# Performance work log

Measured on AMD Instinct MI355X. Metric: run time of the kernel, lower is better.

## Reference

```python
import jax, jax.numpy as jnp
import numpy as np

TOP_K = 1024  # init top_k


def setup_inputs() -> dict:
    key = jax.random.key(0)
    ks = jax.random.split(key, 11)
    B, S, D, H = 8, 1024, 1024, 4096
    s = 0.02
    return {
        "inputs": jax.random.normal(ks[0], (B, S, D), jnp.float32),
        "up_w": jax.random.normal(ks[1], (H, D), jnp.float32) * s,
        "up_b": jax.random.normal(ks[2], (H,), jnp.float32) * s,
        "gate_w1": jax.random.normal(ks[3], (H, D), jnp.float32) * s,
        "gate_b1": jax.random.normal(ks[4], (H,), jnp.float32) * s,
        "gate_w2": jax.random.normal(ks[5], (H, H), jnp.float32) * s,
        "gate_b2": jax.random.normal(ks[6], (H,), jnp.float32) * s,
        "mod_w": jax.random.normal(ks[7], (H, D), jnp.float32) * s,
        "mod_b": jax.random.normal(ks[8], (H,), jnp.float32) * s,
        "down_w": jax.random.normal(ks[9], (D, H), jnp.float32) * s,
        "down_b": jax.random.normal(ks[10], (D,), jnp.float32) * s,
    }


def reference(inputs, up_w, up_b, gate_w1, gate_b1, gate_w2, gate_b2,
              mod_w, mod_b, down_w, down_b):
    B, S, D = inputs.shape
    H = up_w.shape[0]
    # gate: Linear -> ReLU -> Linear, scores [B,S,H]
    scores = jax.nn.relu(jnp.einsum('bsd,hd->bsh', inputs, gate_w1) + gate_b1)
    scores = jnp.einsum('bsh,gh->bsg', scores, gate_w2) + gate_b2
    flat_scores = scores.reshape(B, S * H)
    k = min(TOP_K * S, S * H)
    _, flat_idx = jax.lax.top_k(flat_scores, k)          # [B,k]
    hidden_idx = flat_idx % H                            # [B,k]
    # scatter writes mod.weight[h] at row h -> duplicates harmless -> boolean mask
    batch_idx = jnp.broadcast_to(jnp.arange(B)[:, None], (B, k))
    mask = jnp.zeros((B, H), bool).at[batch_idx, hidden_idx].set(True)
    # per-batch modified weights/bias (materialized like torch repeat+index_put)
    w = jnp.where(mask[:, :, None], mod_w[None], up_w[None])   # [B,H,D]
    b = jnp.where(mask, mod_b[None], up_b[None])               # [B,H]
    h = jnp.einsum('bsd,bhd->bsh', inputs, w) + b[:, None, :]
    h = jax.nn.silu(h)
    # dropout p=0.0 (eval) -> identity
    return jnp.einsum('bsh,dh->bsd', h, down_w) + down_b
```

## Files before the change

### kernel.cpp

```cpp
#include <hip/hip_runtime.h>
#include <cstdint>

typedef __attribute__((ext_vector_type(8))) short short8;
typedef __attribute__((ext_vector_type(4))) float floatx4;
typedef unsigned int uint32;

typedef const void __attribute__((address_space(1)))* gcptr;
typedef void __attribute__((address_space(3)))* lptr;

constexpr int Bn = 8, Sn = 1024, Dn = 1024, Hn = 4096;
constexpr uint32 KTOP = 1024u * 1024u;
constexpr uint32 SKBASE = 0xBB000000u;
constexpr uint32 EMAX = (1u << 27) - 1u;
constexpr uint32 WLO = 3645;
constexpr uint32 WHI = 4157;
constexpr uint32 CAP = 1u << 20;

constexpr size_t NX  = (size_t)Bn * Sn * Dn;
constexpr size_t NW1 = (size_t)Hn * Dn;
constexpr size_t NW2 = (size_t)Hn * Hn;
constexpr size_t NRS = (size_t)Bn * Sn * Hn;

constexpr size_t OFF_XH   = 0;
constexpr size_t OFF_XL   = OFF_XH  + 2 * NX;
constexpr size_t OFF_W1H  = OFF_XL  + 2 * NX;
constexpr size_t OFF_W1L  = OFF_W1H + 2 * NW1;
constexpr size_t OFF_W2H  = OFF_W1L + 2 * NW1;
constexpr size_t OFF_W2L  = OFF_W2H + 2 * NW2;
constexpr size_t OFF_RSH  = OFF_W2L + 2 * NW2;
constexpr size_t OFF_RSL  = OFF_RSH + 2 * NRS;
constexpr size_t OFF_HIST = OFF_RSL + 2 * NRS;
constexpr size_t OFF_HIST2= OFF_HIST + (size_t)Bn * 8192 * 4;
constexpr size_t OFF_HMAX = OFF_HIST2+ (size_t)Bn * 16384 * 4;
constexpr size_t OFF_META = OFF_HMAX + (size_t)Bn * Hn * 4;
constexpr size_t OFF_BSEL = OFF_META + 4096;
constexpr size_t OFF_MASK = OFF_BSEL + (size_t)Bn * Hn * 4;
constexpr size_t WS_SMALL = OFF_MASK + (size_t)Bn * Hn * 4;
constexpr size_t ZERO_BYTES = OFF_BSEL - OFF_HIST;
constexpr size_t OFF_BUF  = OFF_XL;

#define VMCNT(n) asm volatile("s_waitcnt vmcnt(" #n ")" ::: "memory")

__device__ __forceinline__ ushort f2bf(float f) {
  uint32 u = __float_as_uint(f);
  u += 0x7fffu + ((u >> 16) & 1u);
  return (ushort)(u >> 16);
}
__device__ __forceinline__ float bf2f(ushort h) {
  return __uint_as_float(((uint32)h) << 16);
}
__device__ __forceinline__ uint32 skey(float v) {
  uint32 u = __float_as_uint(v);
  return (u & 0x80000000u) ? ~u : (u | 0x80000000u);
}
__device__ __forceinline__ uint32 ekey(uint32 key) {
  if (key <= SKBASE) return 0u;
  uint32 d = key - SKBASE;
  return d > EMAX ? EMAX : d;
}
__device__ __forceinline__ void g2l(const ushort* src, ushort* dst) {
  __builtin_amdgcn_global_load_lds((gcptr)src, (lptr)dst, 16, 0, 0);
}
__device__ __forceinline__ void stage_tile(ushort* lds, const ushort* gbase, int ldg, int tid) {
  const int w = tid >> 6;
  const int c0 = tid, c1 = tid + 256;
  g2l(gbase + (size_t)(c0 >> 2) * ldg + (c0 & 3) * 8, lds + (size_t)(w * 64) * 8);
  g2l(gbase + (size_t)(c1 >> 2) * ldg + (c1 & 3) * 8, lds + (size_t)(256 + w * 64) * 8);
}

__global__ __launch_bounds__(256) void cvt_split_k(const float4* __restrict__ x,
                                                   ushort* __restrict__ hi,
                                                   ushort* __restrict__ lo, int n4) {
  int stride = gridDim.x * 256;
  for (int i = blockIdx.x * 256 + threadIdx.x; i < n4; i += stride) {
    float4 v = x[i];
    ushort h0 = f2bf(v.x), h1 = f2bf(v.y), h2 = f2bf(v.z), h3 = f2bf(v.w);
    ushort4 hv; hv.x = h0; hv.y = h1; hv.z = h2; hv.w = h3;
    *(ushort4*)(hi + (size_t)i * 4) = hv;
    ushort4 lv;
    lv.x = f2bf(v.x - bf2f(h0)); lv.y = f2bf(v.y - bf2f(h1));
    lv.z = f2bf(v.z - bf2f(h2)); lv.w = f2bf(v.w - bf2f(h3));
    *(ushort4*)(lo + (size_t)i * 4) = lv;
  }
}
__global__ __launch_bounds__(256) void cvt_single_k(const float4* __restrict__ x,
                                                    ushort* __restrict__ hi, int n4) {
  int stride = gridDim.x * 256;
  for (int i = blockIdx.x * 256 + threadIdx.x; i < n4; i += stride) {
    float4 v = x[i];
    ushort4 hv; hv.x = f2bf(v.x); hv.y = f2bf(v.y); hv.z = f2bf(v.z); hv.w = f2bf(v.w);
    *(ushort4*)(hi + (size_t)i * 4) = hv;
  }
}
__global__ __launch_bounds__(256) void zero_out_k(float* __restrict__ o, int n) {
  int i = blockIdx.x * 256 + threadIdx.x;
  if (i < n) o[i] = 0.f;
}

constexpr int EPI_RELU = 0;
constexpr int EPI_SCORE = 1;
constexpr int EPI_SILU = 2;
constexpr int EPI_F32 = 3;

template <bool SPLIT, bool SELB, int EPI>
__global__ __launch_bounds__(256, SPLIT ? 3 : 2) void gemm_bt(
    const ushort* __restrict__ Ah, const ushort* __restrict__ Al,
    const ushort* __restrict__ Bh, const ushort* __restrict__ Bl,
    const uint32* __restrict__ bmask,
    int N, int K, long long a_bs, long long o_bs, long long bias_bs,
    const float* __restrict__ bias,
    void* __restrict__ outp, void* __restrict__ out2p) {
  __shared__ __align__(16) ushort lds[SPLIT ? 16384 : 8192];
  ushort* As = lds;
  ushort* Bs = lds + (SPLIT ? 8192 : 4096);

  const int tid = threadIdx.x;
  const int w = tid >> 6, l = tid & 63;
  const int wm = (w >> 1) << 6, wn = (w & 1) << 6;
  const int lm = l & 15, lq = l >> 4;
  const int m0 = blockIdx.y << 7, n0 = blockIdx.x << 7;
  const int z = blockIdx.z;

  const ushort* pAh = Ah + (size_t)z * a_bs + (size_t)m0 * K;
  const ushort* pBh = Bh + (size_t)n0 * K;

  floatx4 acc[4][4];
#pragma unroll
  for (int i = 0; i < 4; i++)
#pragma unroll
    for (int j = 0; j < 4; j++) acc[i][j] = floatx4{0.f, 0.f, 0.f, 0.f};

  for (int k0 = 0; k0 < K; k0 += 32) {
    stage_tile(As, pAh + k0, K, tid);
    stage_tile(Bs, pBh + k0, K, tid);
    __syncthreads();
    short8 afh[4], bfh[4];
#pragma unroll
    for (int i = 0; i < 4; i++)
      afh[i] = *(const short8*)&As[(wm + i * 16 + lm) * 32 + lq * 8];
#pragma unroll
    for (int i = 0; i < 4; i++)
      bfh[i] = *(const short8*)&Bs[(wn + i * 16 + lm) * 32 + lq * 8];
#pragma unroll
    for (int mi = 0; mi < 4; mi++)
#pragma unroll
      for (int ni = 0; ni < 4; ni++)
        acc[mi][ni] = __builtin_amdgcn_mfma_f32_16x16x32_bf16(afh[mi], bfh[ni], acc[mi][ni], 0, 0, 0);
    __syncthreads();
  }

  if constexpr (EPI == EPI_SILU) {
    ushort* o = (ushort*)outp + (size_t)z * o_bs;
    const float* bb = bias + (size_t)z * bias_bs;
#pragma unroll
    for (int mi = 0; mi < 4; mi++)
#pragma unroll
      for (int ni = 0; ni < 4; ni++) {
        int gm = m0 + wm + mi * 16 + lq * 4;
        int gn = n0 + wn + ni * 16 + lm;
        float bnv = bb[gn];
#pragma unroll
        for (int r = 0; r < 4; r++) {
          float v = acc[mi][ni][r] + bnv;
          float s = v / (1.f + __expf(-v));
          o[(size_t)(gm + r) * N + gn] = f2bf(s);
        }
      }
  } else if constexpr (EPI == EPI_F32) {
    float* o = (float*)outp;
#pragma unroll
    for (int mi = 0; mi < 4; mi++)
#pragma unroll
      for (int ni = 0; ni < 4; ni++) {
        int gm = m0 + wm + mi * 16 + lq * 4;
        int gn = n0 + wn + ni * 16 + lm;
        float bnv = bias[gn];
#pragma unroll
        for (int r = 0; r < 4; r++)
          o[(size_t)(gm + r) * N + gn] = acc[mi][ni][r] + bnv;
      }
  }
}

__device__ __forceinline__ short8 fragld(const ushort* S, int r, int swz) {
  return *(const short8*)&S[r * 32 + swz];
}
__device__ __forceinline__ void mfma_block(floatx4 (&acc)[8][4], const short8 (&af)[4],
                                           int mi0, const short8 (&bf)[4]) {
#pragma unroll
  for (int mi = 0; mi < 4; mi++)
#pragma unroll
    for (int ni = 0; ni < 4; ni++)
      acc[mi0 + mi][ni] =
          __builtin_amdgcn_mfma_f32_16x16x32_bf16(af[mi], bf[ni], acc[mi0 + mi][ni], 0, 0, 0);
}

template <bool ST>
__device__ __forceinline__ void kstep_sp(
    floatx4 (&acc)[8][4], ushort* ldsb, int p, int ko,
    const ushort* sAh0, const ushort* sAh1, const ushort* sBh0, const ushort* sBh1,
    const ushort* sAl0, const ushort* sAl1, const ushort* sBl0, const ushort* sBl1,
    int dbase, int swz, int lm, int wrow, int wcol) {
  const ushort* AhS = ldsb + (p * 4 + 0) * 8192;
  const ushort* BhS = ldsb + (p * 4 + 1) * 8192;
  const ushort* AlS = ldsb + (p * 4 + 2) * 8192;
  const ushort* BlS = ldsb + (p * 4 + 3) * 8192;
  ushort* dAh = ldsb + ((p ^ 1) * 4 + 0) * 8192;
  ushort* dBh = ldsb + ((p ^ 1) * 4 + 1) * 8192;
  ushort* dAl = ldsb + ((p ^ 1) * 4 + 2) * 8192;
  ushort* dBl = ldsb + ((p ^ 1) * 4 + 3) * 8192;

  short8 ahT[4], ahB[4], bh[4], bl[4];
#pragma unroll
  for (int i = 0; i < 4; i++) ahT[i] = fragld(AhS, wrow + i * 16 + lm, swz);
#pragma unroll
  for (int i = 0; i < 4; i++) bh[i]  = fragld(BhS, wcol + i * 16 + lm, swz);
#pragma unroll
  for (int i = 0; i < 4; i++) ahB[i] = fragld(AhS, wrow + 64 + i * 16 + lm, swz);
  if constexpr (ST) { g2l(sAh0 + ko, dAh + dbase); g2l(sAh1 + ko, dAh + dbase + 4096); }
  __builtin_amdgcn_s_barrier();
  __builtin_amdgcn_s_setprio(1);
  mfma_block(acc, ahT, 0, bh);
  __builtin_amdgcn_s_setprio(0);
  if constexpr (ST) VMCNT(2); else VMCNT(0);
  __builtin_amdgcn_s_barrier();
#pragma unroll
  for (int i = 0; i < 4; i++) bl[i] = fragld(BlS, wcol + i * 16 + lm, swz);
  if constexpr (ST) { g2l(sBh0 + ko, dBh + dbase); g2l(sBh1 + ko, dBh + dbase + 4096); }
  __builtin_amdgcn_s_barrier();
  __builtin_amdgcn_s_setprio(1);
  mfma_block(acc, ahB, 4, bh);
  __builtin_amdgcn_s_setprio(0);
  __builtin_amdgcn_s_barrier();
  if constexpr (ST) { g2l(sAl0 + ko, dAl + dbase); g2l(sAl1 + ko, dAl + dbase + 4096); }
  __builtin_amdgcn_s_barrier();
  __builtin_amdgcn_s_setprio(1);
  mfma_block(acc, ahT, 0, bl);
  __builtin_amdgcn_s_setprio(0);
  __builtin_amdgcn_s_barrier();
  short8 alT[4];
#pragma unroll
  for (int i = 0; i < 4; i++) alT[i] = fragld(AlS, wrow + i * 16 + lm, swz);
  if constexpr (ST) { g2l(sBl0 + ko, dBl + dbase); g2l(sBl1 + ko, dBl + dbase + 4096); }
  __builtin_amdgcn_s_barrier();
  __builtin_amdgcn_s_setprio(1);
  mfma_block(acc, ahB, 4, bl);
  __builtin_amdgcn_s_setprio(0);
  __builtin_amdgcn_s_barrier();
  short8 alB[4];
#pragma unroll
  for (int i = 0; i < 4; i++) alB[i] = fragld(AlS, wrow + 64 + i * 16 + lm, swz);
  __builtin_amdgcn_s_barrier();
  __builtin_amdgcn_s_setprio(1);
  mfma_block(acc, alT, 0, bh);
  __builtin_amdgcn_s_setprio(0);
  __builtin_amdgcn_s_barrier();
  __builtin_amdgcn_s_setprio(1);
  mfma_block(acc, alB, 4, bh);
  __builtin_amdgcn_s_setprio(0);
  if constexpr (ST) VMCNT(4);
  __builtin_amdgcn_s_barrier();
}

template <bool ST>
__device__ __forceinline__ void kstep_ns(
    floatx4 (&acc)[8][4], ushort* ldsb, int p, int ko,
    const ushort* sA0, const ushort* sA1, const ushort* sB0, const ushort* sB1,
    int dbase, int swz, int lm, int wrow, int wcol) {
  const ushort* AS = ldsb + (p * 2 + 0) * 8192;
  const ushort* BS = ldsb + (p * 2 + 1) * 8192;
  ushort* dA = ldsb + ((p ^ 1) * 2 + 0) * 8192;
  ushort* dB = ldsb + ((p ^ 1) * 2 + 1) * 8192;
  short8 aT[4], aB[4], b[4];
#pragma unroll
  for (int i = 0; i < 4; i++) aT[i] = fragld(AS, wrow + i * 16 + lm, swz);
#pragma unroll
  for (int i = 0; i < 4; i++) b[i]  = fragld(BS, wcol + i * 16 + lm, swz);
#pragma unroll
  for (int i = 0; i < 4; i++) aB[i] = fragld(AS, wrow + 64 + i * 16 + lm, swz);
  if constexpr (ST) {
    g2l(sA0 + ko, dA + dbase); g2l(sA1 + ko, dA + dbase + 4096);
    g2l(sB0 + ko, dB + dbase); g2l(sB1 + ko, dB + dbase + 4096);
  }
  __builtin_amdgcn_s_barrier();
  __builtin_amdgcn_s_setprio(1);
  mfma_block(acc, aT, 0, b);
  __builtin_amdgcn_s_setprio(0);
  __builtin_amdgcn_s_barrier();
  __builtin_amdgcn_s_setprio(1);
  mfma_block(acc, aB, 4, b);
  __builtin_amdgcn_s_setprio(0);
  if constexpr (ST) VMCNT(0);
  __builtin_amdgcn_s_barrier();
}

template <int EPI, bool SPLIT, bool SELB>
__global__ __launch_bounds__(512, 2) void gemm256(
    const ushort* __restrict__ Ah, const ushort* __restrict__ Al,
    const ushort* __restrict__ Bh, const ushort* __restrict__ Bl,
    const uint32* __restrict__ bmask,
    int N, int K, long long a_bs, long long o_bs, long long bias_bs,
    const float* __restrict__ bias,
    ushort* __restrict__ outh, ushort* __restrict__ outl,
    uint32* __restrict__ hist, uint32* __restrict__ hmax,
    uint32* __restrict__ buf, uint32* __restrict__ cnt) {
  static_assert(EPI != EPI_SCORE || SPLIT, "score path is split");
  static_assert(!(SPLIT && SELB), "unused combo");
  constexpr int NSUB = SPLIT ? 4 : 2;
  __shared__ __align__(16) ushort lds[2 * NSUB * 8192];
  ushort* ldsb = &lds[0];

  const int tid = threadIdx.x;
  const int l = tid & 63, w = tid >> 6;
  const int lm = l & 15, lq = l >> 4;
  const int swz = (lq ^ ((lm >> 1) & 3)) << 3;
  const int wrow = (w >> 2) << 7, wcol = (w & 3) << 6;
  const int m0 = blockIdx.y << 8, n0 = blockIdx.x << 8;
  const int z = blockIdx.z;

  const int cg = ((l & 3) ^ ((l >> 3) & 3)) << 3;
  const int r0 = (w << 4) + (l >> 2);
  const size_t soff0 = (size_t)r0 * K + cg;
  const size_t soff1 = soff0 + (size_t)128 * K;
  const int dbase = w << 9;

  const ushort* pA = Ah + (size_t)z * a_bs + (size_t)m0 * K;
  const ushort* sAh0 = pA + soff0;
  const ushort* sAh1 = pA + soff1;
  const ushort* sAl0 = nullptr;
  const ushort* sAl1 = nullptr;
  if constexpr (SPLIT) {
    const ushort* pAl = Al + (size_t)z * a_bs + (size_t)m0 * K;
    sAl0 = pAl + soff0;
    sAl1 = pAl + soff1;
  }
  const ushort* sBh0;
  const ushort* sBh1;
  if constexpr (SELB) {
    const uint32* bm = bmask + (size_t)z * Hn;
    const int gr0 = n0 + r0, gr1 = gr0 + 128;
    sBh0 = (bm[gr0] ? Bl : Bh) + (size_t)gr0 * K + cg;
    sBh1 = (bm[gr1] ? Bl : Bh) + (size_t)gr1 * K + cg;
  } else {
    sBh0 = Bh + (size_t)n0 * K + soff0;
    sBh1 = Bh + (size_t)n0 * K + soff1;
  }
  const ushort* sBl0 = nullptr;
  const ushort* sBl1 = nullptr;
  if constexpr (SPLIT) {
    sBl0 = Bl + (size_t)n0 * K + soff0;
    sBl1 = Bl + (size_t)n0 * K + soff1;
  }

  floatx4 acc[8][4];
#pragma unroll
  for (int i = 0; i < 8; i++)
#pragma unroll
    for (int j = 0; j < 4; j++) acc[i][j] = floatx4{0.f, 0.f, 0.f, 0.f};

  g2l(sAh0, ldsb + 0 * 8192 + dbase); g2l(sAh1, ldsb + 0 * 8192 + dbase + 4096);
  g2l(sBh0, ldsb + 1 * 8192 + dbase); g2l(sBh1, ldsb + 1 * 8192 + dbase + 4096);
  if constexpr (SPLIT) {
    g2l(sAl0, ldsb + 2 * 8192 + dbase); g2l(sAl1, ldsb + 2 * 8192 + dbase + 4096);
    g2l(sBl0, ldsb + 3 * 8192 + dbase); g2l(sBl1, ldsb + 3 * 8192 + dbase + 4096);
    VMCNT(4);
  } else {
    VMCNT(0);
  }
  __builtin_amdgcn_s_barrier();

  const int nk = K >> 5;
  int T = 0;
  for (; T < nk - 1; ++T) {
    const int ko = (T + 1) << 5;
    if constexpr (SPLIT)
      kstep_sp<true>(acc, ldsb, T & 1, ko, sAh0, sAh1, sBh0, sBh1, sAl0, sAl1, sBl0, sBl1,
                     dbase, swz, lm, wrow, wcol);
    else
      kstep_ns<true>(acc, ldsb, T & 1, ko, sAh0, sAh1, sBh0, sBh1,
                     dbase, swz, lm, wrow, wcol);
  }
  if constexpr (SPLIT)
    kstep_sp<false>(acc, ldsb, T & 1, 0, sAh0, sAh1, sBh0, sBh1, sAl0, sAl1, sBl0, sBl1,
                    dbase, swz, lm, wrow, wcol);
  else
    kstep_ns<false>(acc, ldsb, T & 1, 0, sAh0, sAh1, sBh0, sBh1,
                    dbase, swz, lm, wrow, wcol);

  if constexpr (EPI == EPI_RELU) {
#pragma unroll
    for (int mi = 0; mi < 8; mi++)
#pragma unroll
      for (int ni = 0; ni < 4; ni++) {
        const int gm = m0 + wrow + mi * 16 + lq * 4;
        const int gn = n0 + wcol + ni * 16 + lm;
        const float bnv = bias[gn];
#pragma unroll
        for (int r = 0; r < 4; r++) {
          float v = fmaxf(acc[mi][ni][r] + bnv, 0.f);
          ushort h = f2bf(v);
          size_t o = (size_t)(gm + r) * N + gn;
          outh[o] = h;
          outl[o] = f2bf(v - bf2f(h));
        }
      }
  } else if constexpr (EPI == EPI_SILU) {
    ushort* o = outh + (size_t)z * o_bs;
    const float* bb = bias + (size_t)z * bias_bs;
#pragma unroll
    for (int mi = 0; mi < 8; mi++)
#pragma unroll
      for (int ni = 0; ni < 4; ni++) {
        const int gm = m0 + wrow + mi * 16 + lq * 4;
        const int gn = n0 + wcol + ni * 16 + lm;
        const float bnv = bb[gn];
#pragma unroll
        for (int r = 0; r < 4; r++) {
          float v = acc[mi][ni][r] + bnv;
          float s = v / (1.f + __expf(-v));
          o[(size_t)(gm + r) * N + gn] = f2bf(s);
        }
      }
  } else if constexpr (EPI == EPI_SCORE) {
    __syncthreads();
    uint32* hs = (uint32*)ldsb;
    for (int i = tid; i < 8192; i += 512) hs[i] = 0;
    __syncthreads();
    const int batch = m0 >> 10;
    uint32 cntl = 0;
#pragma unroll
    for (int ni = 0; ni < 4; ni++) {
      const int gn = n0 + wcol + ni * 16 + lm;
      const float bnv = bias[gn];
      float vmax = -3.4e38f;
#pragma unroll
      for (int mi = 0; mi < 8; mi++) {
#pragma unroll
        for (int r = 0; r < 4; r++) {
          float v = acc[mi][ni][r] + bnv;
          uint32 e = ekey(skey(v));
          uint32 bk = e >> 14;
          atomicAdd(&hs[bk], 1u);
          if (bk >= WLO && bk <= WHI) cntl++;
          vmax = fmaxf(vmax, v);
        }
      }
      atomicMax(&hmax[batch * Hn + gn], skey(vmax));
    }
    __syncthreads();
    for (int i = tid; i < 8192; i += 512) {
      uint32 c = hs[i];
      if (c) atomicAdd(&hist[batch * 8192 + i], c);
    }
    __syncthreads();
    hs[tid] = cntl;
    __syncthreads();
    if (tid == 0) {
      uint32 run = 0;
      for (int i = 0; i < 512; i++) { uint32 t = hs[i]; hs[i] = run; run += t; }
      hs[512] = atomicAdd(&cnt[batch], run);
    }
    __syncthreads();
    uint32 off = hs[512] + hs[tid];
    uint32* bb = buf + (size_t)batch * CAP;
#pragma unroll
    for (int ni = 0; ni < 4; ni++) {
      const int gn = n0 + wcol + ni * 16 + lm;
      const float bnv = bias[gn];
#pragma unroll
      for (int mi = 0; mi < 8; mi++) {
#pragma unroll
        for (int r = 0; r < 4; r++) {
          float v = acc[mi][ni][r] + bnv;
          uint32 e = ekey(skey(v));
          uint32 bk = e >> 14;
          if (bk >= WLO && bk <= WHI) {
            if (off < CAP) bb[off] = e;
            off++;
          }
        }
      }
    }
  }
}

__global__ __launch_bounds__(256) void select1_k(const uint32* __restrict__ hist,
                                                 uint32* __restrict__ meta) {
  int b = blockIdx.x;
  const uint32* h = hist + b * 8192;
  __shared__ uint32 ps[256];
  uint32 s = 0;
  int base = threadIdx.x * 32;
  for (int i = 0; i < 32; i++) s += h[base + i];
  ps[threadIdx.x] = s;
  __syncthreads();
  if (threadIdx.x == 0) {
    uint32 cum = 0, need = 1;
    int j = 0;
    for (int c = 255; c >= 0; c--) {
      if (cum + ps[c] >= KTOP) {
        for (int i = c * 32 + 31;; i--) {
          uint32 hv = h[i];
          if (cum + hv >= KTOP) { j = i; need = KTOP - cum; break; }
          cum += hv;
        }
        break;
      }
      cum += ps[c];
    }
    meta[8 + b] = (uint32)j;
    meta[16 + b] = need;
    meta[b] = SKBASE + ((uint32)j << 14);
  }
}

__global__ __launch_bounds__(256) void refine_buf_k(const uint32* __restrict__ buf,
                                                    const uint32* __restrict__ meta,
                                                    uint32* __restrict__ hist2) {
  const uint32* cnt = meta + 32;
  size_t stride = (size_t)gridDim.x * 256;
  for (int b = 0; b < Bn; b++) {
    uint32 n = cnt[b] < CAP ? cnt[b] : CAP;
    uint32 j = meta[8 + b];
    const uint32* bb = buf + (size_t)b * CAP;
    for (size_t i = (size_t)blockIdx.x * 256 + threadIdx.x; i < n; i += stride) {
      uint32 e = bb[i];
      if ((e >> 14) == j) atomicAdd(&hist2[(size_t)b * 16384 + (e & 0x3FFFu)], 1u);
    }
  }
}

__global__ __launch_bounds__(256) void select2_k(const uint32* __restrict__ hist2,
                                                 uint32* __restrict__ meta) {
  int b = blockIdx.x;
  const uint32* h2 = hist2 + (size_t)b * 16384;
  __shared__ uint32 ps[256];
  uint32 s = 0;
  const uint32* p = h2 + (size_t)threadIdx.x * 64;
  for (int i = 0; i < 64; i += 4) {
    uint4 v = *(const uint4*)(p + i);
    s += v.x + v.y + v.z + v.w;
  }
  ps[threadIdx.x] = s;
  __syncthreads();
  if (threadIdx.x == 0) {
    uint32 j = meta[8 + b];
    uint32 valid = (j >= WLO && j <= WHI && meta[32 + b] <= CAP) ? 1u : 0u;
    if (valid) {
      uint32 need = meta[16 + b];
      uint32 cum = 0;
      int c = 255;
      for (; c > 0; c--) {
        if (cum + ps[c] >= need) break;
        cum += ps[c];
      }
      uint32 rem = 0;
      for (int i = 63; i >= 0; i--) {
        uint32 hv = h2[c * 64 + i];
        if (cum + hv >= need) { rem = (uint32)(c * 64 + i); break; }
        cum += hv;
      }
      meta[b] = SKBASE + (j << 14) + rem;
    }
  }
}

__global__ __launch_bounds__(256) void mask_k(const uint32* __restrict__ hmax,
                                              const uint32* __restrict__ meta,
                                              const float* __restrict__ modb,
                                              const float* __restrict__ upb,
                                              uint32* __restrict__ mask,
                                              float* __restrict__ bsel) {
  int i = blockIdx.x * 256 + threadIdx.x;
  int b = i >> 12, h = i & 4095;
  bool m = hmax[i] >= meta[b];
  mask[i] = m ? 1u : 0u;
  bsel[i] = m ? modb[h] : upb[h];
}

extern "C" void kernel_launch(void* const* d_in, const int* in_sizes, int n_in,
                              void* d_out, int out_size, void* d_ws, size_t ws_size,
                              hipStream_t stream) {
  (void)in_sizes; (void)n_in;
  const float* x    = (const float*)d_in[0];
  const float* up_w = (const float*)d_in[1];
  const float* up_b = (const float*)d_in[2];
  const float* g_w1 = (const float*)d_in[3];
  const float* g_b1 = (const float*)d_in[4];
  const float* g_w2 = (const float*)d_in[5];
  const float* g_b2 = (const float*)d_in[6];
  const float* mod_w= (const float*)d_in[7];
  const float* mod_b= (const float*)d_in[8];
  const float* dw   = (const float*)d_in[9];
  const float* db   = (const float*)d_in[10];
  float* out = (float*)d_out;

  if (ws_size < WS_SMALL) {
    zero_out_k<<<(out_size + 255) / 256, 256, 0, stream>>>(out, out_size);
    return;
  }

  char* ws = (char*)d_ws;
  ushort* XH  = (ushort*)(ws + OFF_XH);
  ushort* XL  = (ushort*)(ws + OFF_XL);
  ushort* W1H = (ushort*)(ws + OFF_W1H);
  ushort* W1L = (ushort*)(ws + OFF_W1L);
  ushort* W2H = (ushort*)(ws + OFF_W2H);
  ushort* W2L = (ushort*)(ws + OFF_W2L);
  ushort* RSH = (ushort*)(ws + OFF_RSH);
  ushort* RSL = (ushort*)(ws + OFF_RSL);
  uint32* HIST = (uint32*)(ws + OFF_HIST);
  uint32* HIST2= (uint32*)(ws + OFF_HIST2);
  uint32* HMAX = (uint32*)(ws + OFF_HMAX);
  uint32* META = (uint32*)(ws + OFF_META);
  float*  BSEL = (float*)(ws + OFF_BSEL);
  uint32* MASK = (uint32*)(ws + OFF_MASK);
  uint32* BUF  = (uint32*)(ws + OFF_BUF);
  ushort* UPW  = W1H;
  ushort* MODW = W1L;
  ushort* DWNW = XL;
  ushort* HBUF = RSH;

  hipMemsetAsync(ws + OFF_HIST, 0, ZERO_BYTES, stream);

  cvt_split_k<<<1024, 256, 0, stream>>>((const float4*)x, XH, XL, (int)(NX / 4));
  cvt_split_k<<<1024, 256, 0, stream>>>((const float4*)g_w1, W1H, W1L, (int)(NW1 / 4));
  cvt_split_k<<<2048, 256, 0, stream>>>((const float4*)g_w2, W2H, W2L, (int)(NW2 / 4));

  gemm256<EPI_RELU, true, false><<<dim3(Hn / 256, (Bn * Sn) / 256), 512, 0, stream>>>(
      XH, XL, W1H, W1L, nullptr, Hn, Dn, 0, 0, 0, g_b1, RSH, RSL,
      nullptr, nullptr, nullptr, nullptr);
  gemm256<EPI_SCORE, true, false><<<dim3(Hn / 256, (Bn * Sn) / 256), 512, 0, stream>>>(
      RSH, RSL, W2H, W2L, nullptr, Hn, Hn, 0, 0, 0, g_b2, nullptr, nullptr,
      HIST, HMAX, BUF, META + 32);

  select1_k<<<Bn, 256, 0, stream>>>(HIST, META);
  refine_buf_k<<<512, 256, 0, stream>>>(BUF, META, HIST2);
  select2_k<<<Bn, 256, 0, stream>>>(HIST2, META);
  mask_k<<<(Bn * Hn) / 256, 256, 0, stream>>>(HMAX, META, mod_b, up_b, MASK, BSEL);

  cvt_single_k<<<1024, 256, 0, stream>>>((const float4*)up_w, UPW, (int)(NW1 / 4));
  cvt_single_k<<<1024, 256, 0, stream>>>((const float4*)mod_w, MODW, (int)(NW1 / 4));
  cvt_single_k<<<1024, 256, 0, stream>>>((const float4*)dw, DWNW, (int)(NW1 / 4));

  gemm256<EPI_SILU, false, true><<<dim3(Hn / 256, Sn / 256, Bn), 512, 0, stream>>>(
      XH, nullptr, UPW, MODW, MASK, Hn, Dn,
      (long long)Sn * Dn, (long long)Sn * Hn, (long long)Hn,
      BSEL, HBUF, nullptr, nullptr, nullptr, nullptr, nullptr);
  gemm_bt<false, false, EPI_F32><<<dim3(Dn / 128, (Bn * Sn) / 128, 1), 256, 0, stream>>>(
      HBUF, nullptr, DWNW, nullptr, nullptr, Dn, Hn, 0, 0, 0, db, out, nullptr);
}
```

Baseline: 1.256 ms.

## Restructure split-bf16 GEMM k-step into three phases with cross-iteration fragment prefetch

The split (hi/lo bf16) GEMM main loop is reorganised from six barrier-separated MFMA blocks into three phases, each pairing two MFMA blocks. Global-to-LDS copies are issued in larger groups, and sched_barrier fences keep the compiler from reordering them. The next iteration's hi A/B fragments are loaded from the other LDS buffer during the last phase and carried across iterations in registers. This cuts barrier count and hides LDS read latency, at the cost of more live registers and tighter vmcnt accounting that must match the new issue order.

```diff
diff --git a/kernel.cpp b/kernel.cpp
--- a/kernel.cpp
+++ b/kernel.cpp
@@ -40,6 +40,7 @@
 constexpr size_t OFF_BUF  = OFF_XL;
 
 #define VMCNT(n) asm volatile("s_waitcnt vmcnt(" #n ")" ::: "memory")
+#define SCHED0 __builtin_amdgcn_sched_barrier(0)
 
 __device__ __forceinline__ ushort f2bf(float f) {
   uint32 u = __float_as_uint(f);
@@ -196,70 +197,78 @@
 }
 
 template <bool ST>
-__device__ __forceinline__ void kstep_sp(
+__device__ __forceinline__ void kstep3(
     floatx4 (&acc)[8][4], ushort* ldsb, int p, int ko,
     const ushort* sAh0, const ushort* sAh1, const ushort* sBh0, const ushort* sBh1,
     const ushort* sAl0, const ushort* sAl1, const ushort* sBl0, const ushort* sBl1,
-    int dbase, int swz, int lm, int wrow, int wcol) {
+    int dbase, int swz, int lm, int wrow, int wcol,
+    short8 (&ahT)[4], short8 (&bh)[4]) {
+  const int q = p ^ 1;
   const ushort* AhS = ldsb + (p * 4 + 0) * 8192;
-  const ushort* BhS = ldsb + (p * 4 + 1) * 8192;
   const ushort* AlS = ldsb + (p * 4 + 2) * 8192;
   const ushort* BlS = ldsb + (p * 4 + 3) * 8192;
-  ushort* dAh = ldsb + ((p ^ 1) * 4 + 0) * 8192;
-  ushort* dBh = ldsb + ((p ^ 1) * 4 + 1) * 8192;
-  ushort* dAl = ldsb + ((p ^ 1) * 4 + 2) * 8192;
-  ushort* dBl = ldsb + ((p ^ 1) * 4 + 3) * 8192;
-
-  short8 ahT[4], ahB[4], bh[4], bl[4];
-#pragma unroll
-  for (int i = 0; i < 4; i++) ahT[i] = fragld(AhS, wrow + i * 16 + lm, swz);
-#pragma unroll
-  for (int i = 0; i < 4; i++) bh[i]  = fragld(BhS, wcol + i * 16 + lm, swz);
+  ushort* dAh = ldsb + (q * 4 + 0) * 8192;
+  ushort* dBh = ldsb + (q * 4 + 1) * 8192;
+  ushort* dAl = ldsb + (q * 4 + 2) * 8192;
+  ushort* dBl = ldsb + (q * 4 + 3) * 8192;
+
+  short8 ahB[4], bl[4];
+  __builtin_amdgcn_s_barrier();
+  SCHED0;
 #pragma unroll
   for (int i = 0; i < 4; i++) ahB[i] = fragld(AhS, wrow + 64 + i * 16 + lm, swz);
-  if constexpr (ST) { g2l(sAh0 + ko, dAh + dbase); g2l(sAh1 + ko, dAh + dbase + 4096); }
-  __builtin_amdgcn_s_barrier();
+#pragma unroll
+  for (int i = 0; i < 4; i++) bl[i] = fragld(BlS, wcol + i * 16 + lm, swz);
+  if constexpr (ST) {
+    g2l(sAh0 + ko, dAh + dbase); g2l(sAh1 + ko, dAh + dbase + 4096);
+    g2l(sBh0 + ko, dBh + dbase); g2l(sBh1 + ko, dBh + dbase + 4096);
+    g2l(sBl0 + ko, dBl + dbase); g2l(sBl1 + ko, dBl + dbase + 4096);
+  }
+  SCHED0;
   __builtin_amdgcn_s_setprio(1);
   mfma_block(acc, ahT, 0, bh);
-  __builtin_amdgcn_s_setprio(0);
-  if constexpr (ST) VMCNT(2); else VMCNT(0);
-  __builtin_amdgcn_s_barrier();
-#pragma unroll
-  for (int i = 0; i < 4; i++) bl[i] = fragld(BlS, wcol + i * 16 + lm, swz);
-  if constexpr (ST) { g2l(sBh0 + ko, dBh + dbase); g2l(sBh1 + ko, dBh + dbase + 4096); }
-  __builtin_amdgcn_s_barrier();
-  __builtin_amdgcn_s_setprio(1);
   mfma_block(acc, ahB, 4, bh);
   __builtin_amdgcn_s_setprio(0);
+  if constexpr (ST) VMCNT(6); else VMCNT(0);
+
+  short8 alT[4], alB[4];
   __builtin_amdgcn_s_barrier();
-  if constexpr (ST) { g2l(sAl0 + ko, dAl + dbase); g2l(sAl1 + ko, dAl + dbase + 4096); }
-  __builtin_amdgcn_s_barrier();
+  SCHED0;
+#pragma unroll
+  for (int i = 0; i < 4; i++) alT[i] = fragld(AlS, wrow + i * 16 + lm, swz);
+#pragma unroll
+  for (int i = 0; i < 4; i++) alB[i] = fragld(AlS, wrow + 64 + i * 16 + lm, swz);
+  if constexpr (ST) {
+    g2l(sAl0 + ko, dAl + dbase); g2l(sAl1 + ko, dAl + dbase + 4096);
+  }
+  SCHED0;
   __builtin_amdgcn_s_setprio(1);
   mfma_block(acc, ahT, 0, bl);
-  __builtin_amdgcn_s_setprio(0);
-  __builtin_amdgcn_s_barrier();
-  short8 alT[4];
-#pragma unroll
-  for (int i = 0; i < 4; i++) alT[i] = fragld(AlS, wrow + i * 16 + lm, swz);
-  if constexpr (ST) { g2l(sBl0 + ko, dBl + dbase); g2l(sBl1 + ko, dBl + dbase + 4096); }
-  __builtin_amdgcn_s_barrier();
-  __builtin_amdgcn_s_setprio(1);
   mfma_block(acc, ahB, 4, bl);
   __builtin_amdgcn_s_setprio(0);
+  if constexpr (ST) VMCNT(4);
+
   __builtin_amdgcn_s_barrier();
-  short8 alB[4];
-#pragma unroll
-  for (int i = 0; i < 4; i++) alB[i] = fragld(AlS, wrow + 64 + i * 16 + lm, swz);
-  __builtin_amdgcn_s_barrier();
+  SCHED0;
+  short8 ahTn[4], bhn[4];
+  if constexpr (ST) {
+    const ushort* AhSn = ldsb + (q * 4 + 0) * 8192;
+    const ushort* BhSn = ldsb + (q * 4 + 1) * 8192;
+#pragma unroll
+    for (int i = 0; i < 4; i++) ahTn[i] = fragld(AhSn, wrow + i * 16 + lm, swz);
+#pragma unroll
+    for (int i = 0; i < 4; i++) bhn[i] = fragld(BhSn, wcol + i * 16 + lm, swz);
+  }
+  SCHED0;
   __builtin_amdgcn_s_setprio(1);
   mfma_block(acc, alT, 0, bh);
-  __builtin_amdgcn_s_setprio(0);
-  __builtin_amdgcn_s_barrier();
-  __builtin_amdgcn_s_setprio(1);
   mfma_block(acc, alB, 4, bh);
   __builtin_amdgcn_s_setprio(0);
-  if constexpr (ST) VMCNT(4);
-  __builtin_amdgcn_s_barrier();
+  if constexpr (ST) {
+    VMCNT(2);
+#pragma unroll
+    for (int i = 0; i < 4; i++) { ahT[i] = ahTn[i]; bh[i] = bhn[i]; }
+  }
 }
 
 template <bool ST>
@@ -358,34 +367,39 @@
 #pragma unroll
     for (int j = 0; j < 4; j++) acc[i][j] = floatx4{0.f, 0.f, 0.f, 0.f};
 
-  g2l(sAh0, ldsb + 0 * 8192 + dbase); g2l(sAh1, ldsb + 0 * 8192 + dbase + 4096);
-  g2l(sBh0, ldsb + 1 * 8192 + dbase); g2l(sBh1, ldsb + 1 * 8192 + dbase + 4096);
+  const int nk = K >> 5;
+
   if constexpr (SPLIT) {
+    g2l(sAh0, ldsb + 0 * 8192 + dbase); g2l(sAh1, ldsb + 0 * 8192 + dbase + 4096);
+    g2l(sBh0, ldsb + 1 * 8192 + dbase); g2l(sBh1, ldsb + 1 * 8192 + dbase + 4096);
+    g2l(sBl0, ldsb + 3 * 8192 + dbase); g2l(sBl1, ldsb + 3 * 8192 + dbase + 4096);
     g2l(sAl0, ldsb + 2 * 8192 + dbase); g2l(sAl1, ldsb + 2 * 8192 + dbase + 4096);
-    g2l(sBl0, ldsb + 3 * 8192 + dbase); g2l(sBl1, ldsb + 3 * 8192 + dbase + 4096);
-    VMCNT(4);
+    VMCNT(2);
+    __builtin_amdgcn_s_barrier();
+    SCHED0;
+    short8 ahT[4], bh[4];
+#pragma unroll
+    for (int i = 0; i < 4; i++) ahT[i] = fragld(ldsb + 0 * 8192, wrow + i * 16 + lm, swz);
+#pragma unroll
+    for (int i = 0; i < 4; i++) bh[i]  = fragld(ldsb + 1 * 8192, wcol + i * 16 + lm, swz);
+    int T = 0;
+    for (; T < nk - 1; ++T)
+      kstep3<true>(acc, ldsb, T & 1, (T + 1) << 5, sAh0, sAh1, sBh0, sBh1,
+                   sAl0, sAl1, sBl0, sBl1, dbase, swz, lm, wrow, wcol, ahT, bh);
+    kstep3<false>(acc, ldsb, T & 1, 0, sAh0, sAh1, sBh0, sBh1,
+                  sAl0, sAl1, sBl0, sBl1, dbase, swz, lm, wrow, wcol, ahT, bh);
   } else {
+    g2l(sAh0, ldsb + 0 * 8192 + dbase); g2l(sAh1, ldsb + 0 * 8192 + dbase + 4096);
+    g2l(sBh0, ldsb + 1 * 8192 + dbase); g2l(sBh1, ldsb + 1 * 8192 + dbase + 4096);
     VMCNT(0);
-  }
-  __builtin_amdgcn_s_barrier();
-
-  const int nk = K >> 5;
-  int T = 0;
-  for (; T < nk - 1; ++T) {
-    const int ko = (T + 1) << 5;
-    if constexpr (SPLIT)
-      kstep_sp<true>(acc, ldsb, T & 1, ko, sAh0, sAh1, sBh0, sBh1, sAl0, sAl1, sBl0, sBl1,
+    __builtin_amdgcn_s_barrier();
+    int T = 0;
+    for (; T < nk - 1; ++T)
+      kstep_ns<true>(acc, ldsb, T & 1, (T + 1) << 5, sAh0, sAh1, sBh0, sBh1,
                      dbase, swz, lm, wrow, wcol);
-    else
-      kstep_ns<true>(acc, ldsb, T & 1, ko, sAh0, sAh1, sBh0, sBh1,
-                     dbase, swz, lm, wrow, wcol);
-  }
-  if constexpr (SPLIT)
-    kstep_sp<false>(acc, ldsb, T & 1, 0, sAh0, sAh1, sBh0, sBh1, sAl0, sAl1, sBl0, sBl1,
-                    dbase, swz, lm, wrow, wcol);
-  else
     kstep_ns<false>(acc, ldsb, T & 1, 0, sAh0, sAh1, sBh0, sBh1,
                     dbase, swz, lm, wrow, wcol);
+  }
 
   if constexpr (EPI == EPI_RELU) {
 #pragma unroll
```

After: 1.272 ms. About the same (+1.3%).
